# Kernel tuning notes

Measured on AMD Instinct MI355X. Metric: run time of the kernel, lower is better.

Reference implementation:

```python
import jax, jax.numpy as jnp
import numpy as np

N_NODES = 10000
N_EDGES = 640000
FEAT = 128
MID = 128


def setup_inputs() -> dict:
    key = jax.random.key(0)
    ks = jax.random.split(key, 8)
    z = jax.random.normal(ks[0], (N_NODES, FEAT), dtype=jnp.float32)
    scene_attr = jax.random.normal(ks[1], (N_NODES, 16), dtype=jnp.float32)
    graph = jax.random.uniform(ks[2], (N_NODES, N_NODES), dtype=jnp.float32)
    edge_index = jax.random.randint(ks[3], (2, N_EDGES), 0, N_NODES, dtype=jnp.int64)
    s1 = 1.0 / np.sqrt(2 * FEAT + 1)
    s2 = 1.0 / np.sqrt(FEAT)
    s3 = 1.0 / np.sqrt(MID)
    W1 = jax.random.normal(ks[4], (2 * FEAT + 1, FEAT), dtype=jnp.float32) * s1
    W2 = jax.random.normal(ks[5], (FEAT, MID), dtype=jnp.float32) * s2
    W3 = jax.random.normal(ks[6], (MID, MID), dtype=jnp.float32) * s3
    W4 = jax.random.normal(ks[7], (MID, 1), dtype=jnp.float32) * s3
    b1 = jnp.zeros((FEAT,), jnp.float32)
    b2 = jnp.zeros((MID,), jnp.float32)
    b3 = jnp.zeros((MID,), jnp.float32)
    b4 = jnp.zeros((1,), jnp.float32)
    return {"z": z, "scene_attr": scene_attr, "graph": graph, "edge_index": edge_index,
            "W1": W1, "b1": b1, "W2": W2, "b2": b2, "W3": W3, "b3": b3, "W4": W4, "b4": b4}


def reference(z, scene_attr, graph, edge_index, W1, b1, W2, b2, W3, b3, W4, b4):
    src = edge_index[0]  # [E]
    dst = edge_index[1]  # [E]
    # gather: node features of both endpoints + pairwise graph scalar
    g = graph[src, dst][:, None]                      # [E, 1]
    feat = jnp.concatenate([z[src], z[dst], g], axis=-1)  # [E, 2*F+1]
    h = jax.nn.relu(feat @ W1 + b1)
    h = jax.nn.relu(h @ W2 + b2)
    h = jax.nn.relu(h @ W3 + b3)
    value = h @ W4 + b4                               # [E, 1]
    return jax.nn.sigmoid(value)
```

## Files before the change

### kernel.cpp

```cpp
#include <hip/hip_runtime.h>
#include <hip/hip_bf16.h>

typedef short bh8 __attribute__((ext_vector_type(8)));
typedef char  i8x8 __attribute__((ext_vector_type(8)));
typedef char  i8x16 __attribute__((ext_vector_type(16)));
typedef float f32x4 __attribute__((ext_vector_type(4)));

#define NBLOCKS_MAIN 512
#define PNODES 16

__device__ __forceinline__ short f2bf(float f) {
  __hip_bfloat16 h = __float2bfloat16(f);
  return *reinterpret_cast<short*>(&h);
}
__device__ __forceinline__ float bf2f(short s) {
  return __uint_as_float(((uint)(ushort)s) << 16);
}
__device__ __forceinline__ int fpos(int f) {
  int kf = (f >> 5) & 3, h = (f >> 4) & 1, q = (f >> 2) & 3, j = f & 3;
  return (q << 5) | (kf << 3) | (h << 2) | j;
}

__global__ __launch_bounds__(256) void precompute_p(
    const float* __restrict__ z, const float* __restrict__ W1,
    const float* __restrict__ b1, char* __restrict__ Pai,
    char* __restrict__ Pbi, float* __restrict__ Pas, float* __restrict__ Pbs,
    const float* __restrict__ W2, const float* __restrict__ W3,
    ushort* __restrict__ w2f, ushort* __restrict__ w3f,
    int NN, int NPRE) {
  const int tid = threadIdx.x;
  if ((int)blockIdx.x >= NPRE) {
    int idx = ((int)blockIdx.x - NPRE) * 256 + tid;
    if (idx < 16384) {
      int e = idx & 7, l = (idx >> 3) & 63, kb = (idx >> 9) & 3, ob = idx >> 11;
      int qq = l >> 4;
      int k = kb * 32 + (e < 4 ? qq * 4 + e : 16 + qq * 4 + (e - 4));
      int n = ob * 16 + (l & 15);
      w2f[idx] = (ushort)f2bf(W2[k * 128 + n]);
      w3f[idx] = (ushort)f2bf(W3[k * 128 + n]);
    }
    return;
  }
  __shared__ __align__(16) float zs[PNODES][128];
  __shared__ float wmax[4][PNODES];
  const int n0 = blockIdx.x * PNODES;
  for (int i = tid; i < PNODES * 128; i += 256) {
    int m = i >> 7, ff = i & 127, n = n0 + m;
    zs[m][ff] = (n < NN) ? z[(size_t)n * 128 + ff] : 0.f;
  }
  __syncthreads();
  const int f = tid & 127;
  const bool isA = tid < 128;
  const float* w = W1 + (isA ? 0 : 128) * 128 + f;
  const float bias = isA ? b1[f] : 0.f;
  float a[PNODES];
#pragma unroll
  for (int m = 0; m < PNODES; ++m) a[m] = bias;
  for (int k4 = 0; k4 < 32; ++k4) {
    float wv0 = w[(size_t)(k4 * 4 + 0) * 128];
    float wv1 = w[(size_t)(k4 * 4 + 1) * 128];
    float wv2 = w[(size_t)(k4 * 4 + 2) * 128];
    float wv3 = w[(size_t)(k4 * 4 + 3) * 128];
#pragma unroll
    for (int m = 0; m < PNODES; ++m) {
      f32x4 z4 = *(const f32x4*)&zs[m][k4 * 4];
      a[m] = fmaf(z4[0], wv0, a[m]);
      a[m] = fmaf(z4[1], wv1, a[m]);
      a[m] = fmaf(z4[2], wv2, a[m]);
      a[m] = fmaf(z4[3], wv3, a[m]);
    }
  }
  const int wv_ = tid >> 6;
#pragma unroll
  for (int m = 0; m < PNODES; ++m) {
    float v = fabsf(a[m]);
#pragma unroll
    for (int dd = 1; dd < 64; dd <<= 1) v = fmaxf(v, __shfl_xor(v, dd, 64));
    if ((tid & 63) == 0) wmax[wv_][m] = v;
  }
  __syncthreads();
  const int w0 = isA ? 0 : 2;
  char* di = isA ? Pai : Pbi;
  float* ds = isA ? Pas : Pbs;
  const int pos = fpos(f);
#pragma unroll
  for (int m = 0; m < PNODES; ++m) {
    int n = n0 + m;
    if (n < NN) {
      float mx = fmaxf(fmaxf(wmax[w0][m], wmax[w0 + 1][m]), 1e-20f);
      di[(size_t)n * 128 + pos] = (char)(int)rintf(a[m] * (127.0f / mx));
      if (f == 0) ds[n] = mx / 127.0f;
    }
  }
}

struct alignas(16) SMem {
  ushort w2[16384];
  ushort w3[16384];
  float b2[128], b3[128], w4[128];
  ushort w1gp[128];
};

union U16 { i8x16 v; i8x8 h2[2]; };

__global__ __launch_bounds__(256, 2) void edge_mlp(
    const char* __restrict__ Pai, const char* __restrict__ Pbi,
    const float* __restrict__ Pas, const float* __restrict__ Pbs,
    const ushort* __restrict__ w2f, const ushort* __restrict__ w3f,
    const float* __restrict__ graph, const int* __restrict__ ei,
    const float* __restrict__ W1, const float* __restrict__ b2,
    const float* __restrict__ b3, const float* __restrict__ W4,
    const float* __restrict__ b4, float* __restrict__ out, int E, int NN) {
  __shared__ SMem s;
  const int tid = threadIdx.x;
  {
    const uint4* s2 = (const uint4*)w2f;
    const uint4* s3 = (const uint4*)w3f;
    uint4* d2 = (uint4*)s.w2;
    uint4* d3 = (uint4*)s.w3;
    for (int i = tid; i < 2048; i += 256) { d2[i] = s2[i]; d3[i] = s3[i]; }
    if (tid < 128) {
      s.b2[tid] = b2[tid]; s.b3[tid] = b3[tid]; s.w4[tid] = W4[tid];
      s.w1gp[fpos(tid)] = (ushort)f2bf(W1[256 * 128 + tid]);
    }
  }
  __syncthreads();

  const float b4v = b4[0];
  const int lane = tid & 63;
  const int c = lane & 15;
  const int q = lane >> 4;
  const int wgid = (int)blockIdx.x * 4 + (tid >> 6);
  const int n_tiles = (E + 63) / 64;
  const f32x4 z4 = {0.f, 0.f, 0.f, 0.f};

  bh8 w1gb[4];
#pragma unroll
  for (int kf = 0; kf < 4; ++kf)
    w1gb[kf] = *(const bh8*)&s.w1gp[q * 32 + kf * 8];

  for (int tile = wgid; tile < n_tiles; tile += NBLOCKS_MAIN * 4) {
    const int ebase = tile * 64;

    int se[4], de[4];
    float gv[4], sa[4], sb[4];
#pragma unroll
    for (int et = 0; et < 4; ++et) {
      int e = ebase + et * 16 + c;
      if (e >= E) e = E - 1;
      se[et] = __builtin_nontemporal_load(ei + e);
      de[et] = __builtin_nontemporal_load(ei + E + e);
    }
#pragma unroll
    for (int et = 0; et < 4; ++et)
      gv[et] = __builtin_nontemporal_load(graph + (size_t)se[et] * NN + de[et]);
#pragma unroll
    for (int et = 0; et < 4; ++et) {
      sa[et] = Pas[se[et]];
      sb[et] = Pbs[de[et]];
    }

    bh8 bp[4][4];
#pragma unroll
    for (int hp = 0; hp < 2; ++hp) {
      U16 ra2[2][2], rb2[2][2];
#pragma unroll
      for (int e2 = 0; e2 < 2; ++e2) {
        const int et = hp * 2 + e2;
        const char* par = Pai + (size_t)se[et] * 128 + q * 32;
        const char* pbr = Pbi + (size_t)de[et] * 128 + q * 32;
        ra2[e2][0].v = *(const i8x16*)par;  ra2[e2][1].v = *(const i8x16*)(par + 16);
        rb2[e2][0].v = *(const i8x16*)pbr;  rb2[e2][1].v = *(const i8x16*)(pbr + 16);
      }
#pragma unroll
      for (int e2 = 0; e2 < 2; ++e2) {
        const int et = hp * 2 + e2;
        i8x8 pa8[4] = {ra2[e2][0].h2[0], ra2[e2][0].h2[1], ra2[e2][1].h2[0], ra2[e2][1].h2[1]};
        i8x8 pb8[4] = {rb2[e2][0].h2[0], rb2[e2][0].h2[1], rb2[e2][1].h2[0], rb2[e2][1].h2[1]};
#pragma unroll
        for (int kf = 0; kf < 4; ++kf) {
          bh8 t8;
#pragma unroll
          for (int i = 0; i < 8; ++i) {
            float v = fmaf((float)pa8[kf][i], sa[et],
                      fmaf((float)pb8[kf][i], sb[et],
                           gv[et] * bf2f(w1gb[kf][i])));
            t8[i] = f2bf(fmaxf(v, 0.f));
          }
          bp[et][kf] = t8;
        }
      }
      __builtin_amdgcn_sched_barrier(0);
    }

    f32x4 acc[4][8];
#pragma unroll
    for (int et = 0; et < 4; ++et)
#pragma unroll
      for (int ob = 0; ob < 8; ++ob) acc[et][ob] = z4;
#pragma unroll
    for (int kf = 0; kf < 4; ++kf) {
#pragma unroll
      for (int ob = 0; ob < 8; ++ob) {
        bh8 af = *(const bh8*)&s.w2[((ob * 4 + kf) * 64 + lane) * 8];
#pragma unroll
        for (int et = 0; et < 4; ++et)
          acc[et][ob] = __builtin_amdgcn_mfma_f32_16x16x32_bf16(af, bp[et][kf], acc[et][ob], 0, 0, 0);
      }
    }
#pragma unroll
    for (int et = 0; et < 4; ++et) {
#pragma unroll
      for (int kf = 0; kf < 4; ++kf) {
        bh8 t8;
#pragma unroll
        for (int half = 0; half < 2; ++half) {
          int ob = kf * 2 + half;
#pragma unroll
          for (int r = 0; r < 4; ++r) {
            int f = ob * 16 + q * 4 + r;
            float v = fmaxf(acc[et][ob][r] + s.b2[f], 0.f);
            t8[half * 4 + r] = f2bf(v);
          }
        }
        bp[et][kf] = t8;
      }
    }

#pragma unroll
    for (int et = 0; et < 4; ++et)
#pragma unroll
      for (int ob = 0; ob < 8; ++ob) acc[et][ob] = z4;
#pragma unroll
    for (int kf = 0; kf < 4; ++kf) {
#pragma unroll
      for (int ob = 0; ob < 8; ++ob) {
        bh8 af = *(const bh8*)&s.w3[((ob * 4 + kf) * 64 + lane) * 8];
#pragma unroll
        for (int et = 0; et < 4; ++et)
          acc[et][ob] = __builtin_amdgcn_mfma_f32_16x16x32_bf16(af, bp[et][kf], acc[et][ob], 0, 0, 0);
      }
    }

    float psum[4] = {0.f, 0.f, 0.f, 0.f};
#pragma unroll
    for (int et = 0; et < 4; ++et) {
#pragma unroll
      for (int ob = 0; ob < 8; ++ob) {
#pragma unroll
        for (int r = 0; r < 4; ++r) {
          int f = ob * 16 + q * 4 + r;
          float v = fmaxf(acc[et][ob][r] + s.b3[f], 0.f);
          psum[et] += v * s.w4[f];
        }
      }
    }
#pragma unroll
    for (int et = 0; et < 4; ++et) {
      psum[et] += __shfl_xor(psum[et], 16, 64);
      psum[et] += __shfl_xor(psum[et], 32, 64);
    }
    float vsel = (q == 0) ? psum[0] : (q == 1) ? psum[1] : (q == 2) ? psum[2] : psum[3];
    float val = vsel + b4v;
    float sig = 1.0f / (1.0f + __expf(-val));
    int eout = ebase + lane;
    if (eout < E) __builtin_nontemporal_store(sig, out + eout);
  }
}

extern "C" void kernel_launch(void* const* d_in, const int* in_sizes, int n_in,
                              void* d_out, int out_size, void* d_ws, size_t ws_size,
                              hipStream_t stream) {
  const float* z     = (const float*)d_in[0];
  const float* graph = (const float*)d_in[2];
  const int*   ei    = (const int*)d_in[3];
  const float* W1 = (const float*)d_in[4];
  const float* b1 = (const float*)d_in[5];
  const float* W2 = (const float*)d_in[6];
  const float* b2 = (const float*)d_in[7];
  const float* W3 = (const float*)d_in[8];
  const float* b3 = (const float*)d_in[9];
  const float* W4 = (const float*)d_in[10];
  const float* b4 = (const float*)d_in[11];
  int E  = in_sizes[3] / 2;
  int NN = in_sizes[0] / 128;
  int NPRE = (NN + PNODES - 1) / PNODES;

  char* w = (char*)d_ws;
  size_t o = 0;
  auto alloc = [&](size_t bytes) { void* p = w + o; o = (o + bytes + 255) & ~(size_t)255; return p; };
  char*   Pai = (char*)alloc((size_t)NN * 128);
  char*   Pbi = (char*)alloc((size_t)NN * 128);
  float*  Pas = (float*)alloc((size_t)NN * 4);
  float*  Pbs = (float*)alloc((size_t)NN * 4);
  ushort* w2f = (ushort*)alloc(16384 * 2);
  ushort* w3f = (ushort*)alloc(16384 * 2);

  hipLaunchKernelGGL(precompute_p, dim3(NPRE + 64), dim3(256), 0, stream,
                     z, W1, b1, Pai, Pbi, Pas, Pbs, W2, W3, w2f, w3f, NN, NPRE);
  hipLaunchKernelGGL(edge_mlp, dim3(NBLOCKS_MAIN), dim3(256), 0, stream,
                     Pai, Pbi, Pas, Pbs, w2f, w3f, graph, ei,
                     W1, b2, b3, W4, b4, (float*)d_out, E, NN);
}
```

Before: 116.4 us.

## Software-pipeline edge index and graph loads across tiles with lane shuffles

Each lane now loads one edge's src/dst indices and graph scalar for the next tile and the tile after, instead of each lane loading four replicated values per tile. The values are spread to the MFMA lane layout with __shfl. This hides the dependent index-then-graph gather latency behind the current tile's compute and cuts redundant loads. In exchange it adds shuffle instructions and register pressure, and its out-of-range tail clamping makes some loads redundant.

```diff
diff --git a/kernel.cpp b/kernel.cpp
--- a/kernel.cpp
+++ b/kernel.cpp
@@ -130,6 +130,7 @@
   const int lane = tid & 63;
   const int c = lane & 15;
   const int q = lane >> 4;
+  const int STRIDE = NBLOCKS_MAIN * 4;
   const int wgid = (int)blockIdx.x * 4 + (tid >> 6);
   const int n_tiles = (E + 63) / 64;
   const f32x4 z4 = {0.f, 0.f, 0.f, 0.f};
@@ -139,21 +140,44 @@
   for (int kf = 0; kf < 4; ++kf)
     w1gb[kf] = *(const bh8*)&s.w1gp[q * 32 + kf * 8];
 
-  for (int tile = wgid; tile < n_tiles; tile += NBLOCKS_MAIN * 4) {
+  int seA, deA, seB, deB;
+  float gvA;
+  {
+    int eA = wgid * 64 + lane;
+    if (eA >= E) eA = E - 1;
+    if (eA < 0) eA = 0;
+    seA = __builtin_nontemporal_load(ei + eA);
+    deA = __builtin_nontemporal_load(ei + E + eA);
+    gvA = __builtin_nontemporal_load(graph + (size_t)seA * NN + deA);
+    int eB = (wgid + STRIDE) * 64 + lane;
+    if (eB >= E) eB = E - 1;
+    seB = __builtin_nontemporal_load(ei + eB);
+    deB = __builtin_nontemporal_load(ei + E + eB);
+  }
+
+  for (int tile = wgid; tile < n_tiles; tile += STRIDE) {
     const int ebase = tile * 64;
 
     int se[4], de[4];
     float gv[4], sa[4], sb[4];
 #pragma unroll
     for (int et = 0; et < 4; ++et) {
-      int e = ebase + et * 16 + c;
-      if (e >= E) e = E - 1;
-      se[et] = __builtin_nontemporal_load(ei + e);
-      de[et] = __builtin_nontemporal_load(ei + E + e);
-    }
-#pragma unroll
-    for (int et = 0; et < 4; ++et)
-      gv[et] = __builtin_nontemporal_load(graph + (size_t)se[et] * NN + de[et]);
+      int src = et * 16 + c;
+      se[et] = __shfl(seA, src, 64);
+      de[et] = __shfl(deA, src, 64);
+      gv[et] = __shfl(gvA, src, 64);
+    }
+
+    {
+      float gvB = __builtin_nontemporal_load(graph + (size_t)seB * NN + deB);
+      int e2 = (tile + 2 * STRIDE) * 64 + lane;
+      if (e2 >= E) e2 = E - 1;
+      int se2 = __builtin_nontemporal_load(ei + e2);
+      int de2 = __builtin_nontemporal_load(ei + E + e2);
+      seA = seB; deA = deB; gvA = gvB;
+      seB = se2; deB = de2;
+    }
+
 #pragma unroll
     for (int et = 0; et < 4; ++et) {
       sa[et] = Pas[se[et]];
```

Result: slower. 130.6 us (+12.2%).
